# Performance work log

Measured on AMD Instinct MI355X. Metric: run time of the kernel, lower is better.

Reference implementation:

```python
import jax, jax.numpy as jnp
import numpy as np

EMBED_DIM = 1024
NUM_HEADS = 16
HEAD_DIM = EMBED_DIM // NUM_HEADS
SCALE = HEAD_DIM ** -0.5


def setup_inputs() -> dict:
    key = jax.random.key(0)
    ks = jax.random.split(key, 12)
    B, T, S, C = 4, 2048, 2048, EMBED_DIM
    inp = {
        "query": jax.random.normal(ks[0], (B, T, C), dtype=jnp.float32),
        "key": jax.random.normal(ks[1], (B, S, C), dtype=jnp.float32),
        "value": jax.random.normal(ks[2], (B, S, C), dtype=jnp.float32),
        "attn_mask": jnp.zeros((T, S), dtype=jnp.float32),
        "key_padding_mask": jnp.zeros((B, S), dtype=bool),
    }
    std = C ** -0.5
    for i, name in enumerate(["q", "k", "v", "out"]):
        inp[f"W{name}"] = jax.random.normal(ks[3 + i], (C, C), dtype=jnp.float32) * std
        inp[f"b{name}"] = jnp.zeros((C,), dtype=jnp.float32)
    return inp


def reference(query, key, value, attn_mask, key_padding_mask,
              Wq, bq, Wk, bk, Wv, bv, Wout, bout):
    B, T, C = query.shape
    S = key.shape[1]
    H, D = NUM_HEADS, HEAD_DIM
    # linear projections (torch Linear: x @ W.T + b)
    q = (query @ Wq.T + bq).reshape(B, T, H, D).transpose(0, 2, 1, 3)  # (B,H,T,D)
    k = (key @ Wk.T + bk).reshape(B, S, H, D).transpose(0, 2, 1, 3)    # (B,H,S,D)
    v = (value @ Wv.T + bv).reshape(B, S, H, D).transpose(0, 2, 1, 3)  # (B,H,S,D)
    # scaled dot-product attention with full (B,H,T,S) scores (faithful to source)
    scores = jnp.einsum("bhtd,bhsd->bhts", q, k) * SCALE
    scores = scores + attn_mask[None, None, :, :]
    scores = jnp.where(key_padding_mask[:, None, None, :], -jnp.inf, scores)
    weights = jax.nn.softmax(scores, axis=-1)
    attn_out = jnp.einsum("bhts,bhsd->bhtd", weights, v)
    attn_out = attn_out.transpose(0, 2, 1, 3).reshape(B, T, C)
    return attn_out @ Wout.T + bout
```

## Files before the change

kernel.cpp:

```cpp
#include <hip/hip_runtime.h>
#include <stdint.h>

#define NB 4
#define NT 2048
#define NC 1024
#define NH 16
#define ND 64
#define ACT_ELEMS (8388608ull)
#define W_ELEMS   (1048576ull)

typedef __attribute__((ext_vector_type(8))) short short8;
typedef __attribute__((ext_vector_type(4))) float f32x4;
typedef __attribute__((ext_vector_type(2))) unsigned int u32x2;

__device__ __forceinline__ unsigned short f2bf(float x) {
    unsigned int u = __float_as_uint(x);
    u += 0x7fffu + ((u >> 16) & 1u);
    return (unsigned short)(u >> 16);
}
__device__ __forceinline__ unsigned int f2bf2(float a, float b) {
    return (unsigned int)f2bf(a) | ((unsigned int)f2bf(b) << 16);
}

#if defined(__has_builtin)
#if __has_builtin(__builtin_amdgcn_global_load_lds)
#define HAS_GLDS 1
#endif
#endif

__device__ __forceinline__ void gl_lds16(const unsigned short* g, unsigned short* lds_wave_base) {
#ifdef HAS_GLDS
    __builtin_amdgcn_global_load_lds(
        (const __attribute__((address_space(1))) void*)g,
        (__attribute__((address_space(3))) void*)lds_wave_base, 16, 0, 0);
#else
    int lane = threadIdx.x & 63;
    *(short8*)(lds_wave_base + lane * 8) = *(const short8*)g;
#endif
}

__global__ __launch_bounds__(256) void cvt_weights(const float* __restrict__ w0,
                                                   const float* __restrict__ w1,
                                                   const float* __restrict__ w2,
                                                   const float* __restrict__ w3,
                                                   unsigned short* __restrict__ dst) {
    int bid = blockIdx.x;
    int which = bid >> 10;
    const float* src = (which == 0) ? w0 : (which == 1) ? w1 : (which == 2) ? w2 : w3;
    int i = ((bid & 1023) * 256 + threadIdx.x) * 4;
    f32x4 f = *(const f32x4*)(src + i);
    u32x2 pk = {f2bf2(f[0], f[1]), f2bf2(f[2], f[3])};
    *(u32x2*)(dst + (size_t)which * W_ELEMS + i) = pk;
}

template <int MODE>
__device__ __forceinline__ void gemm_body(const float* __restrict__ Af,
                                          const unsigned short* __restrict__ Ab,
                                          const unsigned short* __restrict__ W,
                                          const float* __restrict__ bias,
                                          unsigned short* __restrict__ dstb,
                                          float* __restrict__ dstf) {
    __shared__ unsigned short As[128 * 40];
    __shared__ unsigned short Bs[128 * 32];

    const int tid  = threadIdx.x;
    const int m0   = blockIdx.x * 128;
    const int n0   = blockIdx.y * 128;
    const int lane = tid & 63;
    const int wave = tid >> 6;
    const int col  = lane & 15;
    const int quad = lane >> 4;
    const int wr   = wave >> 1;
    const int wc   = wave & 1;
    const int ASTR = (MODE == 0) ? 40 : 32;

    const int srow = tid >> 2;
    const int skc  = (tid & 3) * 8;

    f32x4 acc[4][4];
    const f32x4 fzero = {0.f, 0.f, 0.f, 0.f};
#pragma unroll
    for (int i = 0; i < 4; ++i)
#pragma unroll
        for (int j = 0; j < 4; ++j) acc[i][j] = fzero;

    for (int k0 = 0; k0 < NC; k0 += 32) {
#pragma unroll
        for (int r = 0; r < 2; ++r) {
            int g   = r * 256 + tid;
            int row = g >> 2;
            int cc  = (g & 3) * 8;
            unsigned short* bbase = Bs + (size_t)(r * 2048 + wave * 512);
            gl_lds16(W + (size_t)(n0 + row) * NC + k0 + cc, bbase);
            if (MODE == 1) {
                unsigned short* abase = As + (size_t)(r * 2048 + wave * 512);
                gl_lds16(Ab + (size_t)(m0 + row) * NC + k0 + cc, abase);
            }
        }
        if (MODE == 0) {
#pragma unroll
            for (int c = 0; c < 2; ++c) {
                int row = srow + c * 64;
                const float* ap = Af + (size_t)(m0 + row) * NC + k0 + skc;
                f32x4 f0 = *(const f32x4*)ap;
                f32x4 f1 = *(const f32x4*)(ap + 4);
                short8 hv;
#pragma unroll
                for (int u = 0; u < 4; ++u) {
                    hv[u]     = (short)f2bf(f0[u]);
                    hv[u + 4] = (short)f2bf(f1[u]);
                }
                *(short8*)&As[row * 40 + skc] = hv;
            }
        }
        __syncthreads();

        short8 af[4], bf[4];
#pragma unroll
        for (int i = 0; i < 4; ++i)
            af[i] = *(const short8*)&As[(wr * 64 + i * 16 + col) * ASTR + quad * 8];
#pragma unroll
        for (int j = 0; j < 4; ++j)
            bf[j] = *(const short8*)&Bs[(wc * 64 + j * 16 + col) * 32 + quad * 8];
#pragma unroll
        for (int i = 0; i < 4; ++i)
#pragma unroll
            for (int j = 0; j < 4; ++j)
                acc[i][j] = __builtin_amdgcn_mfma_f32_16x16x32_bf16(af[i], bf[j], acc[i][j], 0, 0, 0);
        __syncthreads();
    }

#pragma unroll
    for (int j = 0; j < 4; ++j) {
        int n = n0 + wc * 64 + j * 16 + col;
        float bv = bias[n];
#pragma unroll
        for (int i = 0; i < 4; ++i) {
#pragma unroll
            for (int r = 0; r < 4; ++r) {
                int m = m0 + wr * 64 + i * 16 + quad * 4 + r;
                float val = acc[i][j][r] + bv;
                if (MODE == 0) {
                    size_t idx = ((size_t)((m >> 11) * NH + (n >> 6)) * NT + (m & 2047)) * ND + (n & 63);
                    dstb[idx] = f2bf(val);
                } else {
                    dstf[(size_t)m * NC + n] = val;
                }
            }
        }
    }
}

__global__ __launch_bounds__(256) void proj_kernel(const float* __restrict__ x0,
                                                   const float* __restrict__ x1,
                                                   const float* __restrict__ x2,
                                                   const unsigned short* __restrict__ w0,
                                                   const unsigned short* __restrict__ w1,
                                                   const unsigned short* __restrict__ w2,
                                                   const float* __restrict__ b0,
                                                   const float* __restrict__ b1,
                                                   const float* __restrict__ b2,
                                                   unsigned short* __restrict__ qkv) {
    int z = blockIdx.z;
    const float* A          = (z == 0) ? x0 : (z == 1) ? x1 : x2;
    const unsigned short* W = (z == 0) ? w0 : (z == 1) ? w1 : w2;
    const float* bias       = (z == 0) ? b0 : (z == 1) ? b1 : b2;
    gemm_body<0>(A, nullptr, W, bias, qkv + (size_t)z * ACT_ELEMS, nullptr);
}

__global__ __launch_bounds__(256) void outproj_kernel(const unsigned short* __restrict__ ao,
                                                      const unsigned short* __restrict__ w,
                                                      const float* __restrict__ bias,
                                                      float* __restrict__ out) {
    gemm_body<1>(nullptr, ao, w, bias, nullptr, out);
}

__global__ __launch_bounds__(256) void attn_kernel(const unsigned short* __restrict__ q,
                                                   const unsigned short* __restrict__ k,
                                                   const unsigned short* __restrict__ v,
                                                   const float* __restrict__ amask,
                                                   const unsigned char* __restrict__ kpm,
                                                   unsigned short* __restrict__ ao) {
    __shared__ unsigned short Ks[64 * 72];
    __shared__ unsigned short Vt[64 * 72];
    __shared__ unsigned short Pl[4][32 * 72];

    const int tid  = threadIdx.x;
    const int lane = tid & 63;
    const int wave = tid >> 6;
    const int col  = lane & 15;
    const int quad = lane >> 4;

    const int b  = blockIdx.z;
    const int h  = blockIdx.y;
    const int t0 = blockIdx.x * 128;

    const size_t headbase = (size_t)(b * NH + h) * NT * ND;

    short8 qf[2][2];
#pragma unroll
    for (int tg = 0; tg < 2; ++tg) {
        const unsigned short* qr =
            q + headbase + (size_t)(t0 + wave * 32 + tg * 16 + col) * ND + quad * 8;
        qf[tg][0] = *(const short8*)qr;
        qf[tg][1] = *(const short8*)(qr + 32);
    }

    const f32x4 fzero = {0.f, 0.f, 0.f, 0.f};
    f32x4 O[2][4];
#pragma unroll
    for (int tg = 0; tg < 2; ++tg)
#pragma unroll
        for (int dg = 0; dg < 4; ++dg) O[tg][dg] = fzero;
    float lsum[2] = {0.f, 0.f};

    const int ksr = tid >> 2;
    const int ksc = (tid & 3) * 8;
    const int vsp = tid & 31;
    const int vd0 = (tid >> 5) * 8;
    unsigned short* Plw = Pl[wave];

    for (int s0 = 0; s0 < NT; s0 += 64) {
        {
            const unsigned short* kp_ = k + headbase + (size_t)(s0 + ksr) * ND;
            *(short8*)&Ks[ksr * 72 + ksc]      = *(const short8*)(kp_ + ksc);
            *(short8*)&Ks[ksr * 72 + ksc + 32] = *(const short8*)(kp_ + ksc + 32);
        }
        {
            int s_ = vsp * 2;
            const unsigned short* vp = v + headbase + (size_t)(s0 + s_) * ND + vd0;
            short8 va = *(const short8*)vp;
            short8 vb = *(const short8*)(vp + ND);
            unsigned int* dst = (unsigned int*)Vt;
#pragma unroll
            for (int i = 0; i < 8; ++i) {
                unsigned int pk = (unsigned int)(unsigned short)va[i] |
                                  ((unsigned int)(unsigned short)vb[i] << 16);
                dst[(vd0 + i) * 36 + vsp] = pk;
            }
        }
        __syncthreads();

#pragma unroll
        for (int sg = 0; sg < 4; ++sg) {
            const unsigned short* kb_ = &Ks[(sg * 16 + col) * 72 + quad * 8];
            short8 af0 = *(const short8*)kb_;
            short8 af1 = *(const short8*)(kb_ + 32);
            unsigned int kb = *(const unsigned int*)(kpm + b * NT + s0 + sg * 16 + quad * 4);
#pragma unroll
            for (int tg = 0; tg < 2; ++tg) {
                f32x4 z = fzero;
                z = __builtin_amdgcn_mfma_f32_16x16x32_bf16(af0, qf[tg][0], z, 0, 0, 0);
                z = __builtin_amdgcn_mfma_f32_16x16x32_bf16(af1, qf[tg][1], z, 0, 0, 0);
                int t = t0 + wave * 32 + tg * 16 + col;
                f32x4 mv = *(const f32x4*)(amask + (size_t)t * NT + s0 + sg * 16 + quad * 4);
                float p[4];
#pragma unroll
                for (int r = 0; r < 4; ++r) {
                    float scv = z[r] * 0.125f + mv[r];
                    if ((kb >> (r * 8)) & 0xffu) scv = -INFINITY;
                    p[r] = __expf(scv);
                }
                lsum[tg] += (p[0] + p[1]) + (p[2] + p[3]);
                u32x2 pkv;
                pkv[0] = f2bf2(p[0], p[1]);
                pkv[1] = f2bf2(p[2], p[3]);
                *(u32x2*)&Plw[(tg * 16 + col) * 72 + sg * 16 + quad * 4] = pkv;
            }
        }

        short8 pf[2][2];
#pragma unroll
        for (int tg = 0; tg < 2; ++tg)
#pragma unroll
            for (int sk = 0; sk < 2; ++sk)
                pf[tg][sk] = *(const short8*)&Plw[(tg * 16 + col) * 72 + sk * 32 + quad * 8];
#pragma unroll
        for (int dg = 0; dg < 4; ++dg) {
            short8 vf0 = *(const short8*)&Vt[(dg * 16 + col) * 72 + quad * 8];
            short8 vf1 = *(const short8*)&Vt[(dg * 16 + col) * 72 + 32 + quad * 8];
#pragma unroll
            for (int tg = 0; tg < 2; ++tg) {
                O[tg][dg] = __builtin_amdgcn_mfma_f32_16x16x32_bf16(pf[tg][0], vf0, O[tg][dg], 0, 0, 0);
                O[tg][dg] = __builtin_amdgcn_mfma_f32_16x16x32_bf16(pf[tg][1], vf1, O[tg][dg], 0, 0, 0);
            }
        }
        __syncthreads();
    }

    float linv[2];
#pragma unroll
    for (int tg = 0; tg < 2; ++tg) {
        float s = lsum[tg];
        s += __shfl_xor(s, 16);
        s += __shfl_xor(s, 32);
        linv[tg] = 1.0f / s;
    }
#pragma unroll
    for (int tg = 0; tg < 2; ++tg) {
#pragma unroll
        for (int r = 0; r < 4; ++r) {
            float inv = __shfl(linv[tg], quad * 4 + r);
            int t = t0 + wave * 32 + tg * 16 + quad * 4 + r;
#pragma unroll
            for (int dg = 0; dg < 4; ++dg) {
                size_t idx = (size_t)(b * NT + t) * NC + h * ND + dg * 16 + col;
                ao[idx] = f2bf(O[tg][dg][r] * inv);
            }
        }
    }
}

extern "C" void kernel_launch(void* const* d_in, const int* in_sizes, int n_in,
                              void* d_out, int out_size, void* d_ws, size_t ws_size,
                              hipStream_t stream) {
    const float* query = (const float*)d_in[0];
    const float* key_  = (const float*)d_in[1];
    const float* value = (const float*)d_in[2];
    const float* amask = (const float*)d_in[3];
    const unsigned char* kpm = (const unsigned char*)d_in[4];
    const float* Wq = (const float*)d_in[5];
    const float* bq = (const float*)d_in[6];
    const float* Wk = (const float*)d_in[7];
    const float* bk = (const float*)d_in[8];
    const float* Wv = (const float*)d_in[9];
    const float* bv = (const float*)d_in[10];
    const float* Wo = (const float*)d_in[11];
    const float* bo = (const float*)d_in[12];
    float* out = (float*)d_out;

    unsigned short* ws = (unsigned short*)d_ws;
    unsigned short* qb  = ws;
    unsigned short* aob = ws + 3 * ACT_ELEMS;
    unsigned short* wqb = ws + 4 * ACT_ELEMS;
    unsigned short* wkb = wqb + W_ELEMS;
    unsigned short* wvb = wqb + 2 * W_ELEMS;
    unsigned short* wob = wqb + 3 * W_ELEMS;

    cvt_weights<<<4096, 256, 0, stream>>>(Wq, Wk, Wv, Wo, wqb);

    dim3 pg(64, 8, 3);
    proj_kernel<<<pg, 256, 0, stream>>>(query, key_, value, wqb, wkb, wvb, bq, bk, bv, qb);

    dim3 ag(NT / 128, NH, NB);
    attn_kernel<<<ag, 256, 0, stream>>>(qb, qb + ACT_ELEMS, qb + 2 * ACT_ELEMS,
                                        amask, kpm, aob);

    dim3 og(64, 8, 1);
    outproj_kernel<<<og, 256, 0, stream>>>(aob, wob, bo, out);
}
```

Measured before the change: 466.5 us.

## Pre-convert activations to bf16 and double attention query tile per block

Adds a single conversion kernel that turns query/key/value and all weights into bf16 up front. The projection GEMM can then load A tiles straight into LDS with global_load_lds instead of converting fp32 inside the K loop. Separately, the attention kernel now processes 256 query rows per block (64 per wave, enlarged P buffer), halving the number of K/V tile loads per query and adding a 2-blocks-per-CU launch bound. The cost is an extra fp32 read plus bf16 write pass over the activations, and higher register and LDS pressure in the attention kernel.

```diff
diff --git a/kernel.cpp b/kernel.cpp
--- a/kernel.cpp
+++ b/kernel.cpp
@@ -39,28 +39,44 @@
 #endif
 }
 
-__global__ __launch_bounds__(256) void cvt_weights(const float* __restrict__ w0,
-                                                   const float* __restrict__ w1,
-                                                   const float* __restrict__ w2,
-                                                   const float* __restrict__ w3,
-                                                   unsigned short* __restrict__ dst) {
+__global__ __launch_bounds__(256) void cvt_all(const float* __restrict__ q,
+                                               const float* __restrict__ k,
+                                               const float* __restrict__ v,
+                                               const float* __restrict__ wq,
+                                               const float* __restrict__ wk,
+                                               const float* __restrict__ wv,
+                                               const float* __restrict__ wo,
+                                               unsigned short* __restrict__ xb,
+                                               unsigned short* __restrict__ wb) {
     int bid = blockIdx.x;
-    int which = bid >> 10;
-    const float* src = (which == 0) ? w0 : (which == 1) ? w1 : (which == 2) ? w2 : w3;
-    int i = ((bid & 1023) * 256 + threadIdx.x) * 4;
-    f32x4 f = *(const f32x4*)(src + i);
-    u32x2 pk = {f2bf2(f[0], f[1]), f2bf2(f[2], f[3])};
-    *(u32x2*)(dst + (size_t)which * W_ELEMS + i) = pk;
-}
-
-template <int MODE>
-__device__ __forceinline__ void gemm_body(const float* __restrict__ Af,
-                                          const unsigned short* __restrict__ Ab,
+    const float* src;
+    unsigned short* dst;
+    int chunk;
+    if (bid < 12288) {
+        int z = bid >> 12; chunk = bid & 4095;
+        src = (z == 0) ? q : (z == 1) ? k : v;
+        dst = xb + (size_t)z * ACT_ELEMS;
+    } else {
+        int z = (bid - 12288) >> 9; chunk = (bid - 12288) & 511;
+        src = (z == 0) ? wq : (z == 1) ? wk : (z == 2) ? wv : wo;
+        dst = wb + (size_t)z * W_ELEMS;
+    }
+    size_t i = (size_t)chunk * 2048 + (size_t)threadIdx.x * 8;
+    f32x4 f0 = *(const f32x4*)(src + i);
+    f32x4 f1 = *(const f32x4*)(src + i + 4);
+    u32x2 p0 = {f2bf2(f0[0], f0[1]), f2bf2(f0[2], f0[3])};
+    u32x2 p1 = {f2bf2(f1[0], f1[1]), f2bf2(f1[2], f1[3])};
+    *(u32x2*)(dst + i) = p0;
+    *(u32x2*)(dst + i + 4) = p1;
+}
+
+template <int STORE>
+__device__ __forceinline__ void gemm_body(const unsigned short* __restrict__ A,
                                           const unsigned short* __restrict__ W,
                                           const float* __restrict__ bias,
                                           unsigned short* __restrict__ dstb,
                                           float* __restrict__ dstf) {
-    __shared__ unsigned short As[128 * 40];
+    __shared__ unsigned short As[128 * 32];
     __shared__ unsigned short Bs[128 * 32];
 
     const int tid  = threadIdx.x;
@@ -72,10 +88,6 @@
     const int quad = lane >> 4;
     const int wr   = wave >> 1;
     const int wc   = wave & 1;
-    const int ASTR = (MODE == 0) ? 40 : 32;
-
-    const int srow = tid >> 2;
-    const int skc  = (tid & 3) * 8;
 
     f32x4 acc[4][4];
     const f32x4 fzero = {0.f, 0.f, 0.f, 0.f};
@@ -90,35 +102,17 @@
             int g   = r * 256 + tid;
             int row = g >> 2;
             int cc  = (g & 3) * 8;
+            unsigned short* abase = As + (size_t)(r * 2048 + wave * 512);
             unsigned short* bbase = Bs + (size_t)(r * 2048 + wave * 512);
+            gl_lds16(A + (size_t)(m0 + row) * NC + k0 + cc, abase);
             gl_lds16(W + (size_t)(n0 + row) * NC + k0 + cc, bbase);
-            if (MODE == 1) {
-                unsigned short* abase = As + (size_t)(r * 2048 + wave * 512);
-                gl_lds16(Ab + (size_t)(m0 + row) * NC + k0 + cc, abase);
-            }
-        }
-        if (MODE == 0) {
-#pragma unroll
-            for (int c = 0; c < 2; ++c) {
-                int row = srow + c * 64;
-                const float* ap = Af + (size_t)(m0 + row) * NC + k0 + skc;
-                f32x4 f0 = *(const f32x4*)ap;
-                f32x4 f1 = *(const f32x4*)(ap + 4);
-                short8 hv;
-#pragma unroll
-                for (int u = 0; u < 4; ++u) {
-                    hv[u]     = (short)f2bf(f0[u]);
-                    hv[u + 4] = (short)f2bf(f1[u]);
-                }
-                *(short8*)&As[row * 40 + skc] = hv;
-            }
         }
         __syncthreads();
 
         short8 af[4], bf[4];
 #pragma unroll
         for (int i = 0; i < 4; ++i)
-            af[i] = *(const short8*)&As[(wr * 64 + i * 16 + col) * ASTR + quad * 8];
+            af[i] = *(const short8*)&As[(wr * 64 + i * 16 + col) * 32 + quad * 8];
 #pragma unroll
         for (int j = 0; j < 4; ++j)
             bf[j] = *(const short8*)&Bs[(wc * 64 + j * 16 + col) * 32 + quad * 8];
@@ -140,7 +134,7 @@
             for (int r = 0; r < 4; ++r) {
                 int m = m0 + wr * 64 + i * 16 + quad * 4 + r;
                 float val = acc[i][j][r] + bv;
-                if (MODE == 0) {
+                if (STORE == 0) {
                     size_t idx = ((size_t)((m >> 11) * NH + (n >> 6)) * NT + (m & 2047)) * ND + (n & 63);
                     dstb[idx] = f2bf(val);
                 } else {
@@ -151,39 +145,34 @@
     }
 }
 
-__global__ __launch_bounds__(256) void proj_kernel(const float* __restrict__ x0,
-                                                   const float* __restrict__ x1,
-                                                   const float* __restrict__ x2,
-                                                   const unsigned short* __restrict__ w0,
-                                                   const unsigned short* __restrict__ w1,
-                                                   const unsigned short* __restrict__ w2,
+__global__ __launch_bounds__(256) void proj_kernel(const unsigned short* __restrict__ xb,
+                                                   const unsigned short* __restrict__ wb,
                                                    const float* __restrict__ b0,
                                                    const float* __restrict__ b1,
                                                    const float* __restrict__ b2,
                                                    unsigned short* __restrict__ qkv) {
     int z = blockIdx.z;
-    const float* A          = (z == 0) ? x0 : (z == 1) ? x1 : x2;
-    const unsigned short* W = (z == 0) ? w0 : (z == 1) ? w1 : w2;
-    const float* bias       = (z == 0) ? b0 : (z == 1) ? b1 : b2;
-    gemm_body<0>(A, nullptr, W, bias, qkv + (size_t)z * ACT_ELEMS, nullptr);
+    const float* bias = (z == 0) ? b0 : (z == 1) ? b1 : b2;
+    gemm_body<0>(xb + (size_t)z * ACT_ELEMS, wb + (size_t)z * W_ELEMS, bias,
+                 qkv + (size_t)z * ACT_ELEMS, nullptr);
 }
 
 __global__ __launch_bounds__(256) void outproj_kernel(const unsigned short* __restrict__ ao,
                                                       const unsigned short* __restrict__ w,
                                                       const float* __restrict__ bias,
                                                       float* __restrict__ out) {
-    gemm_body<1>(nullptr, ao, w, bias, nullptr, out);
-}
-
-__global__ __launch_bounds__(256) void attn_kernel(const unsigned short* __restrict__ q,
-                                                   const unsigned short* __restrict__ k,
-                                                   const unsigned short* __restrict__ v,
-                                                   const float* __restrict__ amask,
-                                                   const unsigned char* __restrict__ kpm,
-                                                   unsigned short* __restrict__ ao) {
+    gemm_body<1>(ao, w, bias, nullptr, out);
+}
+
+__global__ __launch_bounds__(256, 2) void attn_kernel(const unsigned short* __restrict__ q,
+                                                      const unsigned short* __restrict__ k,
+                                                      const unsigned short* __restrict__ v,
+                                                      const float* __restrict__ amask,
+                                                      const unsigned char* __restrict__ kpm,
+                                                      unsigned short* __restrict__ ao) {
     __shared__ unsigned short Ks[64 * 72];
     __shared__ unsigned short Vt[64 * 72];
-    __shared__ unsigned short Pl[4][32 * 72];
+    __shared__ unsigned short Pl[4][64 * 72];
 
     const int tid  = threadIdx.x;
     const int lane = tid & 63;
@@ -193,26 +182,26 @@
 
     const int b  = blockIdx.z;
     const int h  = blockIdx.y;
-    const int t0 = blockIdx.x * 128;
+    const int t0 = blockIdx.x * 256;
 
     const size_t headbase = (size_t)(b * NH + h) * NT * ND;
 
-    short8 qf[2][2];
-#pragma unroll
-    for (int tg = 0; tg < 2; ++tg) {
+    short8 qf[4][2];
+#pragma unroll
+    for (int tg = 0; tg < 4; ++tg) {
         const unsigned short* qr =
-            q + headbase + (size_t)(t0 + wave * 32 + tg * 16 + col) * ND + quad * 8;
+            q + headbase + (size_t)(t0 + wave * 64 + tg * 16 + col) * ND + quad * 8;
         qf[tg][0] = *(const short8*)qr;
         qf[tg][1] = *(const short8*)(qr + 32);
     }
 
     const f32x4 fzero = {0.f, 0.f, 0.f, 0.f};
-    f32x4 O[2][4];
-#pragma unroll
-    for (int tg = 0; tg < 2; ++tg)
+    f32x4 O[4][4];
+#pragma unroll
+    for (int tg = 0; tg < 4; ++tg)
 #pragma unroll
         for (int dg = 0; dg < 4; ++dg) O[tg][dg] = fzero;
-    float lsum[2] = {0.f, 0.f};
+    float lsum[4] = {0.f, 0.f, 0.f, 0.f};
 
     const int ksr = tid >> 2;
     const int ksc = (tid & 3) * 8;
@@ -248,11 +237,11 @@
             short8 af1 = *(const short8*)(kb_ + 32);
             unsigned int kb = *(const unsigned int*)(kpm + b * NT + s0 + sg * 16 + quad * 4);
 #pragma unroll
-            for (int tg = 0; tg < 2; ++tg) {
+            for (int tg = 0; tg < 4; ++tg) {
                 f32x4 z = fzero;
                 z = __builtin_amdgcn_mfma_f32_16x16x32_bf16(af0, qf[tg][0], z, 0, 0, 0);
                 z = __builtin_amdgcn_mfma_f32_16x16x32_bf16(af1, qf[tg][1], z, 0, 0, 0);
-                int t = t0 + wave * 32 + tg * 16 + col;
+                int t = t0 + wave * 64 + tg * 16 + col;
                 f32x4 mv = *(const f32x4*)(amask + (size_t)t * NT + s0 + sg * 16 + quad * 4);
                 float p[4];
 #pragma unroll
@@ -269,9 +258,9 @@
             }
         }
 
-        short8 pf[2][2];
-#pragma unroll
-        for (int tg = 0; tg < 2; ++tg)
+        short8 pf[4][2];
+#pragma unroll
+        for (int tg = 0; tg < 4; ++tg)
 #pragma unroll
             for (int sk = 0; sk < 2; ++sk)
                 pf[tg][sk] = *(const short8*)&Plw[(tg * 16 + col) * 72 + sk * 32 + quad * 8];
@@ -280,7 +269,7 @@
             short8 vf0 = *(const short8*)&Vt[(dg * 16 + col) * 72 + quad * 8];
             short8 vf1 = *(const short8*)&Vt[(dg * 16 + col) * 72 + 32 + quad * 8];
 #pragma unroll
-            for (int tg = 0; tg < 2; ++tg) {
+            for (int tg = 0; tg < 4; ++tg) {
                 O[tg][dg] = __builtin_amdgcn_mfma_f32_16x16x32_bf16(pf[tg][0], vf0, O[tg][dg], 0, 0, 0);
                 O[tg][dg] = __builtin_amdgcn_mfma_f32_16x16x32_bf16(pf[tg][1], vf1, O[tg][dg], 0, 0, 0);
             }
@@ -288,20 +277,20 @@
         __syncthreads();
     }
 
-    float linv[2];
-#pragma unroll
-    for (int tg = 0; tg < 2; ++tg) {
+    float linv[4];
+#pragma unroll
+    for (int tg = 0; tg < 4; ++tg) {
         float s = lsum[tg];
         s += __shfl_xor(s, 16);
         s += __shfl_xor(s, 32);
         linv[tg] = 1.0f / s;
     }
 #pragma unroll
-    for (int tg = 0; tg < 2; ++tg) {
+    for (int tg = 0; tg < 4; ++tg) {
 #pragma unroll
         for (int r = 0; r < 4; ++r) {
             float inv = __shfl(linv[tg], quad * 4 + r);
-            int t = t0 + wave * 32 + tg * 16 + quad * 4 + r;
+            int t = t0 + wave * 64 + tg * 16 + quad * 4 + r;
 #pragma unroll
             for (int dg = 0; dg < 4; ++dg) {
                 size_t idx = (size_t)(b * NT + t) * NC + h * ND + dg * 16 + col;
@@ -330,22 +319,20 @@
     float* out = (float*)d_out;
 
     unsigned short* ws = (unsigned short*)d_ws;
-    unsigned short* qb  = ws;
-    unsigned short* aob = ws + 3 * ACT_ELEMS;
-    unsigned short* wqb = ws + 4 * ACT_ELEMS;
-    unsigned short* wkb = wqb + W_ELEMS;
-    unsigned short* wvb = wqb + 2 * W_ELEMS;
-    unsigned short* wob = wqb + 3 * W_ELEMS;
-
-    cvt_weights<<<4096, 256, 0, stream>>>(Wq, Wk, Wv, Wo, wqb);
+    unsigned short* xb  = ws;
+    unsigned short* qb  = ws + 3 * ACT_ELEMS;
+    unsigned short* wb  = ws + 6 * ACT_ELEMS;
+    unsigned short* aob = xb;
+
+    cvt_all<<<14336, 256, 0, stream>>>(query, key_, value, Wq, Wk, Wv, Wo, xb, wb);
 
     dim3 pg(64, 8, 3);
-    proj_kernel<<<pg, 256, 0, stream>>>(query, key_, value, wqb, wkb, wvb, bq, bk, bv, qb);
-
-    dim3 ag(NT / 128, NH, NB);
+    proj_kernel<<<pg, 256, 0, stream>>>(xb, wb, bq, bk, bv, qb);
+
+    dim3 ag(NT / 256, NH, NB);
     attn_kernel<<<ag, 256, 0, stream>>>(qb, qb + ACT_ELEMS, qb + 2 * ACT_ELEMS,
                                         amask, kpm, aob);
 
     dim3 og(64, 8, 1);
-    outproj_kernel<<<og, 256, 0, stream>>>(aob, wob, bo, out);
-}
+    outproj_kernel<<<og, 256, 0, stream>>>(aob, wb + 3 * W_ELEMS, bo, out);
+}
```

Measured after the change: 453.6 us. 2.8% less time.
